# Kernel tuning notes

Hardware: AMD Instinct MI355X
Metric: run time of the kernel (lower is better)

The kernel has to match this reference:

```python
import jax, jax.numpy as jnp
import numpy as np

D = 256; NH = 8; NL = 4; NP = 4; NLAYERS = 6; DFF = 1024; DH = D // NH
B = 2
SHAPES = [(128, 128), (64, 64), (32, 32), (16, 16)]
S_TOTAL = sum(h * w for h, w in SHAPES)  # 21760


def setup_inputs() -> dict:
    key = jax.random.key(0)
    ks = iter(jax.random.split(key, 64))
    inp = {}
    for l, (h, w) in enumerate(SHAPES):
        inp[f"src{l}"] = jax.random.normal(next(ks), (B, D, h, w), jnp.float32)
        inp[f"pos{l}"] = jax.random.normal(next(ks), (B, D, h, w), jnp.float32)
    def p(shape):
        return jax.random.normal(next(ks), shape, jnp.float32) * 0.02
    inp["level_embed"] = p((NL, D))
    inp["Woff"] = p((NLAYERS, D, NH * NL * NP * 2)); inp["boff"] = p((NLAYERS, NH * NL * NP * 2))
    inp["Wattn"] = p((NLAYERS, D, NH * NL * NP)); inp["battn"] = p((NLAYERS, NH * NL * NP))
    inp["Wval"] = p((NLAYERS, D, D)); inp["bval"] = p((NLAYERS, D))
    inp["Wout"] = p((NLAYERS, D, D)); inp["bout"] = p((NLAYERS, D))
    inp["ln1_s"] = jnp.ones((NLAYERS, D)); inp["ln1_b"] = jnp.zeros((NLAYERS, D))
    inp["W1"] = p((NLAYERS, D, DFF)); inp["b1"] = p((NLAYERS, DFF))
    inp["W2"] = p((NLAYERS, DFF, D)); inp["b2"] = p((NLAYERS, D))
    inp["ln2_s"] = jnp.ones((NLAYERS, D)); inp["ln2_b"] = jnp.zeros((NLAYERS, D))
    return inp


def _layer_norm(x, s, b, eps=1e-5):
    m = jnp.mean(x, -1, keepdims=True)
    v = jnp.mean((x - m) ** 2, -1, keepdims=True)
    return (x - m) * jax.lax.rsqrt(v + eps) * s + b


def _ref_points(batch):
    # masks are all-False -> valid_ratios == 1, so reference points are just
    # normalized pixel centers, identical across the level axis.
    refs = []
    for h, w in SHAPES:
        yy, xx = jnp.meshgrid((jnp.arange(h) + 0.5) / h, (jnp.arange(w) + 0.5) / w, indexing="ij")
        refs.append(jnp.stack([xx.ravel(), yy.ravel()], -1))
    ref = jnp.concatenate(refs, 0)  # [S, 2] (x, y)
    return jnp.broadcast_to(ref[None, :, None, :], (batch, S_TOTAL, NL, 2))


def _ms_deform_attn(query, ref, src, Woff, boff, Wattn, battn, Wval, bval, Wout, bout):
    Bq, S, _ = query.shape
    value = (src @ Wval + bval).reshape(Bq, S, NH, DH)
    off = (query @ Woff + boff).reshape(Bq, S, NH, NL, NP, 2)
    aw = jax.nn.softmax((query @ Wattn + battn).reshape(Bq, S, NH, NL * NP), -1)
    aw = aw.reshape(Bq, S, NH, NL, NP)
    norm = jnp.array([[w, h] for h, w in SHAPES], dtype=query.dtype)  # [NL,2] = (W,H)
    loc = ref[:, :, None, :, None, :] + off / norm[None, None, None, :, None, :]  # [B,S,NH,NL,NP,2]
    out = jnp.zeros((Bq, NH, S, DH), query.dtype)
    start = 0
    for l, (h, w) in enumerate(SHAPES):
        v = value[:, start:start + h * w].transpose(0, 2, 1, 3)  # [B,NH,h*w,DH]
        start += h * w
        # grid_sample align_corners=False convention
        x = loc[:, :, :, l, :, 0] * w - 0.5  # [B,S,NH,NP]
        y = loc[:, :, :, l, :, 1] * h - 0.5
        x0 = jnp.floor(x); y0 = jnp.floor(y)
        lx = x - x0; ly = y - y0
        x0i = x0.astype(jnp.int32); y0i = y0.astype(jnp.int32)
        def tr(a):  # [B,S,NH,NP] -> [B,NH,S*NP,1]
            return a.transpose(0, 2, 1, 3).reshape(Bq, NH, S * NP, 1)
        def gather(xi, yi):
            ok = (xi >= 0) & (xi < w) & (yi >= 0) & (yi < h)
            idx = jnp.clip(yi, 0, h - 1) * w + jnp.clip(xi, 0, w - 1)
            idx = idx.transpose(0, 2, 1, 3).reshape(Bq, NH, S * NP)
            g = jnp.take_along_axis(v, idx[..., None], axis=2)  # [B,NH,S*NP,DH]
            return g * tr(ok).astype(v.dtype)  # zero padding outside
        samp = (tr((1 - lx) * (1 - ly)) * gather(x0i, y0i)
                + tr(lx * (1 - ly)) * gather(x0i + 1, y0i)
                + tr((1 - lx) * ly) * gather(x0i, y0i + 1)
                + tr(lx * ly) * gather(x0i + 1, y0i + 1))
        samp = (samp * tr(aw[:, :, :, l])).reshape(Bq, NH, S, NP, DH).sum(3)
        out = out + samp
    out = out.transpose(0, 2, 1, 3).reshape(Bq, S, D)
    return out @ Wout + bout


def _forward(srcs, poss, level_embed, Woff, boff, Wattn, battn, Wval, bval, Wout, bout,
             ln1_s, ln1_b, W1, b1, W2, b2, ln2_s, ln2_b):
    bsz = srcs[0].shape[0]
    src_flat = jnp.concatenate([s.reshape(bsz, D, -1).transpose(0, 2, 1) for s in srcs], 1)
    pos_flat = jnp.concatenate(
        [p.reshape(bsz, D, -1).transpose(0, 2, 1) + level_embed[l] for l, p in enumerate(poss)], 1)
    ref = _ref_points(bsz)
    out = src_flat
    for i in range(NLAYERS):
        q = out + pos_flat
        attn = _ms_deform_attn(q, ref, out, Woff[i], boff[i], Wattn[i], battn[i],
                               Wval[i], bval[i], Wout[i], bout[i])
        out = _layer_norm(out + attn, ln1_s[i], ln1_b[i])
        ff = jax.nn.relu(out @ W1[i] + b1[i]) @ W2[i] + b2[i]
        out = _layer_norm(out + ff, ln2_s[i], ln2_b[i])
    return out  # memory: [B, S_TOTAL, D]


def reference(src0, src1, src2, src3, pos0, pos1, pos2, pos3, level_embed,
              Woff, boff, Wattn, battn, Wval, bval, Wout, bout,
              ln1_s, ln1_b, W1, b1, W2, b2, ln2_s, ln2_b):
    return _forward([src0, src1, src2, src3], [pos0, pos1, pos2, pos3], level_embed,
                    Woff, boff, Wattn, battn, Wval, bval, Wout, bout,
                    ln1_s, ln1_b, W1, b1, W2, b2, ln2_s, ln2_b)
```

## Files before the change

kernel.cpp:

```cpp
#include <hip/hip_runtime.h>
#include <math.h>

#define DMODEL 256
#define NHEADS 8
#define NLAY 6
#define DFF 1024
#define DHEAD 32
#define NB 2
#define STOT 21760
#define MTOT (NB * STOT)

typedef unsigned short u16;
typedef __attribute__((ext_vector_type(8))) short short8;
typedef __attribute__((ext_vector_type(4))) float floatx4;
typedef __attribute__((ext_vector_type(2))) float float2v;

__device__ __forceinline__ float bf2f(u16 h) {
    unsigned int u = ((unsigned int)h) << 16;
    return __uint_as_float(u);
}
__device__ __forceinline__ u16 f2bf(float f) {
    unsigned int u = __float_as_uint(f);
    u = u + 0x7fffu + ((u >> 16) & 1u);
    return (u16)(u >> 16);
}

__device__ __forceinline__ void pkfma(float2v& acc, float2v a, float2v b) {
    asm("v_pk_fma_f32 %0, %1, %2, %0" : "+v"(acc) : "v"(a), "v"(b));
}
__device__ __forceinline__ float2v unpk(unsigned int u) {
    float2v r;
    r.x = __uint_as_float(u << 16);
    r.y = __uint_as_float(u & 0xffff0000u);
    return r;
}

__global__ __launch_bounds__(256)
void biascat_kernel(const float* __restrict__ boff, const float* __restrict__ battn,
                    float* __restrict__ bias384)
{
    const int t = blockIdx.x * 256 + threadIdx.x;
    if (t >= NLAY * 384) return;
    const int i = t / 384, c = t - i * 384;
    bias384[t] = (c < 256) ? boff[i * 256 + c] : battn[i * 128 + (c - 256)];
}

__global__ __launch_bounds__(256)
void wtrans_kernel(const float* __restrict__ W, u16* __restrict__ Wt,
                   const int K, const int N, const long wstride, const long ostride)
{
    __shared__ float ts[32][33];
    W  += blockIdx.z * wstride;
    Wt += blockIdx.z * ostride;
    const int n0 = blockIdx.x * 32;
    const int k0 = blockIdx.y * 32;
    const int t = threadIdx.x;
    const int nl = t & 31, kl = t >> 5;
#pragma unroll
    for (int p = 0; p < 4; ++p) {
        const int k = kl + p * 8;
        ts[k][nl] = W[(long)(k0 + k) * N + n0 + nl];
    }
    __syncthreads();
    const int c = t & 31, r0 = t >> 5;
#pragma unroll
    for (int p = 0; p < 4; ++p) {
        const int r = r0 + p * 8;
        Wt[(long)(n0 + r) * K + k0 + c] = f2bf(ts[c][r]);
    }
}

__global__ __launch_bounds__(256)
void flatten_kernel(const float* __restrict__ src, const float* __restrict__ pos,
                    const float* __restrict__ le_row,
                    float* __restrict__ out, u16* __restrict__ outb,
                    u16* __restrict__ posb, u16* __restrict__ qb,
                    int HW, int start)
{
    __shared__ float ts[32][33];
    __shared__ float tp[32][33];
    const int b   = blockIdx.z;
    const int d0  = blockIdx.y * 32;
    const int hw0 = blockIdx.x * 32;
    const int t   = threadIdx.x;
    const int hwl = t & 31;
    const int dl  = t >> 5;
#pragma unroll
    for (int p = 0; p < 4; ++p) {
        const int dd = dl + p * 8;
        const int d  = d0 + dd;
        const long idx = ((long)(b * DMODEL + d)) * HW + hw0 + hwl;
        ts[dd][hwl] = src[idx];
        tp[dd][hwl] = pos[idx] + le_row[d];
    }
    __syncthreads();
    const int dl2  = t & 31;
    const int hwl2 = t >> 5;
#pragma unroll
    for (int p = 0; p < 4; ++p) {
        const int hh  = hwl2 + p * 8;
        const int tok = start + hw0 + hh;
        const long o  = ((long)(b * STOT + tok)) * DMODEL + d0 + dl2;
        const float v = ts[dl2][hh];
        const float pp = tp[dl2][hh];
        out[o]  = v;
        outb[o] = f2bf(v);
        posb[o] = f2bf(pp);
        qb[o]   = f2bf(v + pp);
    }
}

__global__ __launch_bounds__(256)
void mfma_gemm(const u16* __restrict__ A, const u16* __restrict__ Bt,
               const int ldb, const float* __restrict__ bias,
               u16* __restrict__ Cb, const int ldc, u16* __restrict__ Cb2,
               const int K, const int relu)
{
    __shared__ u16 As[128 * 40];
    __shared__ u16 Bs[128 * 40];
    const int tid  = threadIdx.x;
    const int wv   = tid >> 6;
    const int lane = tid & 63;
    const int m0 = blockIdx.y * 128;
    const int n0 = blockIdx.x * 128;
    const int wm = (wv & 1) * 64;
    const int wn = (wv >> 1) * 64;
    const int q   = lane >> 4;
    const int c16 = lane & 15;

    const int srow = tid >> 2;
    const int scol = (tid & 3) * 8;

    floatx4 acc[4][4];
#pragma unroll
    for (int i = 0; i < 4; ++i)
#pragma unroll
        for (int j = 0; j < 4; ++j)
            acc[i][j] = (floatx4){0.f, 0.f, 0.f, 0.f};

    union Frag { short8 v; uint2 u[2]; };

    for (int k0 = 0; k0 < K; k0 += 32) {
#pragma unroll
        for (int it = 0; it < 2; ++it) {
            const int r = srow + it * 64;
            const uint4 va = *(const uint4*)(A + (long)(m0 + r) * K + k0 + scol);
            uint2 lo, hi;
            lo.x = va.x; lo.y = va.y; hi.x = va.z; hi.y = va.w;
            *(uint2*)&As[r * 40 + scol]     = lo;
            *(uint2*)&As[r * 40 + scol + 4] = hi;
            const uint4 vb = *(const uint4*)(Bt + (long)(n0 + r) * ldb + k0 + scol);
            lo.x = vb.x; lo.y = vb.y; hi.x = vb.z; hi.y = vb.w;
            *(uint2*)&Bs[r * 40 + scol]     = lo;
            *(uint2*)&Bs[r * 40 + scol + 4] = hi;
        }
        __syncthreads();

        short8 af[4], bf[4];
#pragma unroll
        for (int i = 0; i < 4; ++i) {
            Frag fa;
            const int ao = (wm + i * 16 + c16) * 40 + q * 8;
            fa.u[0] = *(const uint2*)&As[ao];
            fa.u[1] = *(const uint2*)&As[ao + 4];
            af[i] = fa.v;
            Frag fb;
            const int bo = (wn + i * 16 + c16) * 40 + q * 8;
            fb.u[0] = *(const uint2*)&Bs[bo];
            fb.u[1] = *(const uint2*)&Bs[bo + 4];
            bf[i] = fb.v;
        }
#pragma unroll
        for (int i = 0; i < 4; ++i)
#pragma unroll
            for (int j = 0; j < 4; ++j)
                acc[i][j] = __builtin_amdgcn_mfma_f32_16x16x32_bf16(
                    af[i], bf[j], acc[i][j], 0, 0, 0);
        __syncthreads();
    }

    u16* cb  = Cb;
    int ldcb = ldc, csub = 0;
    if (Cb2 && n0 >= 256) { cb = Cb2; ldcb = 128; csub = 256; }

#pragma unroll
    for (int i = 0; i < 4; ++i) {
#pragma unroll
        for (int j = 0; j < 4; ++j) {
            const int col = n0 + wn + j * 16 + c16;
            const float bv = bias ? bias[col] : 0.f;
#pragma unroll
            for (int r = 0; r < 4; ++r) {
                const int row = m0 + wm + i * 16 + q * 4 + r;
                float v = acc[i][j][r] + bv;
                if (relu) v = fmaxf(v, 0.f);
                cb[(long)row * ldcb + col - csub] = f2bf(v);
            }
        }
    }
}

__device__ __forceinline__ void point_corners(
    float refx, float refy, unsigned int o2, float aP,
    int k, unsigned int base, float w[4], unsigned int o[4])
{
    const int lw = 128 >> k;
    const float flw = (float)lw;
    const float x = refx * flw - 0.5f + bf2f((u16)(o2 & 0xffffu));
    const float y = refy * flw - 0.5f + bf2f((u16)(o2 >> 16));
    const float x0f = floorf(x), y0f = floorf(y);
    const float lx = x - x0f, ly = y - y0f;
    const int x0 = (int)x0f, y0 = (int)y0f;
    const float wx0 = ((unsigned int)x0 < (unsigned int)lw) ? (1.f - lx) : 0.f;
    const float wx1 = ((unsigned int)(x0 + 1) < (unsigned int)lw) ? lx : 0.f;
    const float wy0 = ((unsigned int)y0 < (unsigned int)lw) ? (aP * (1.f - ly)) : 0.f;
    const float wy1 = ((unsigned int)(y0 + 1) < (unsigned int)lw) ? (aP * ly) : 0.f;
    const unsigned int xc0 = (unsigned int)(x0 & (lw - 1)) << 9;
    const unsigned int xc1 = (unsigned int)((x0 + 1) & (lw - 1)) << 9;
    const unsigned int r0 = (unsigned int)(y0 & (lw - 1)) << (16 - k);
    const unsigned int r1 = (unsigned int)((y0 + 1) & (lw - 1)) << (16 - k);
    w[0] = wy0 * wx0; o[0] = base + r0 + xc0;
    w[1] = wy0 * wx1; o[1] = base + r0 + xc1;
    w[2] = wy1 * wx0; o[2] = base + r1 + xc0;
    w[3] = wy1 * wx1; o[3] = base + r1 + xc1;
}

__device__ __forceinline__ void corner_acc(const char* __restrict__ vp,
                                           unsigned int o, float w,
                                           float2v acc[16])
{
    const uint4 d0 = *(const uint4*)(vp + o);
    const uint4 d1 = *(const uint4*)(vp + o + 16);
    const uint4 d2 = *(const uint4*)(vp + o + 32);
    const uint4 d3 = *(const uint4*)(vp + o + 48);
    float2v w2; w2.x = w; w2.y = w;
    pkfma(acc[0],  w2, unpk(d0.x));
    pkfma(acc[1],  w2, unpk(d0.y));
    pkfma(acc[2],  w2, unpk(d0.z));
    pkfma(acc[3],  w2, unpk(d0.w));
    pkfma(acc[4],  w2, unpk(d1.x));
    pkfma(acc[5],  w2, unpk(d1.y));
    pkfma(acc[6],  w2, unpk(d1.z));
    pkfma(acc[7],  w2, unpk(d1.w));
    pkfma(acc[8],  w2, unpk(d2.x));
    pkfma(acc[9],  w2, unpk(d2.y));
    pkfma(acc[10], w2, unpk(d2.z));
    pkfma(acc[11], w2, unpk(d2.w));
    pkfma(acc[12], w2, unpk(d3.x));
    pkfma(acc[13], w2, unpk(d3.y));
    pkfma(acc[14], w2, unpk(d3.z));
    pkfma(acc[15], w2, unpk(d3.w));
}

__global__ __launch_bounds__(256)
void sample_kernel(const u16* __restrict__ value, const u16* __restrict__ offb,
                   const u16* __restrict__ logit, u16* __restrict__ sb)
{
    __shared__ float red[4][64][33];

    const int t  = threadIdx.x;
    const int wv = t >> 6;
    const int l  = t & 63;
    const int h  = l >> 3;
    const int q  = l & 7;
    const int blk = blockIdx.x * 4 + wv;
    const int b = blk / STOT;
    const int s = blk - b * STOT;

    float refx, refy;
    if (s < 16384) {
        const int yy = s >> 7, xx = s & 127;
        refx = (xx + 0.5f) * (1.f / 128.f); refy = (yy + 0.5f) * (1.f / 128.f);
    } else if (s < 20480) {
        const int sl = s - 16384; const int yy = sl >> 6, xx = sl & 63;
        refx = (xx + 0.5f) * (1.f / 64.f);  refy = (yy + 0.5f) * (1.f / 64.f);
    } else if (s < 21504) {
        const int sl = s - 20480; const int yy = sl >> 5, xx = sl & 31;
        refx = (xx + 0.5f) * (1.f / 32.f);  refy = (yy + 0.5f) * (1.f / 32.f);
    } else {
        const int sl = s - 21504; const int yy = sl >> 4, xx = sl & 15;
        refx = (xx + 0.5f) * (1.f / 16.f);  refy = (yy + 0.5f) * (1.f / 16.f);
    }

    const unsigned int* offp = (const unsigned int*)(offb + (long)blk * 256 + h * 32);
    const unsigned int o2_0 = offp[q];
    const unsigned int o2_1 = offp[q + 8];
    const u16* lp = logit + (long)blk * 128 + h * 16;
    const float l0 = bf2f(lp[q]);
    const float l1 = bf2f(lp[q + 8]);

    float m = fmaxf(l0, l1);
    m = fmaxf(m, __shfl_xor(m, 1));
    m = fmaxf(m, __shfl_xor(m, 2));
    m = fmaxf(m, __shfl_xor(m, 4));
    const float e0 = __expf(l0 - m);
    const float e1 = __expf(l1 - m);
    float se = e0 + e1;
    se += __shfl_xor(se, 1);
    se += __shfl_xor(se, 2);
    se += __shfl_xor(se, 4);
    const float inv = 1.f / se;
    const float aP0 = e0 * inv;
    const float aP1 = e1 * inv;

    const int k0 = q >> 2;
    const int k1 = k0 + 2;
    const unsigned int LS0 = k0 ? 16384u : 0u;
    const unsigned int LS1 = k0 ? 21504u : 20480u;
    const unsigned int tb = (unsigned int)(b * STOT);
    const unsigned int hb64 = (unsigned int)(h * 64);
    const unsigned int base0 = (tb + LS0) * 512u + hb64;
    const unsigned int base1 = (tb + LS1) * 512u + hb64;

    float w0[4], w1[4];
    unsigned int oo0[4], oo1[4];
    point_corners(refx, refy, o2_0, aP0, k0, base0, w0, oo0);
    point_corners(refx, refy, o2_1, aP1, k1, base1, w1, oo1);

    float2v acc[16];
#pragma unroll
    for (int n = 0; n < 16; ++n) { acc[n].x = 0.f; acc[n].y = 0.f; }

    const char* vp = (const char*)value;
#pragma unroll
    for (int c = 0; c < 4; ++c) corner_acc(vp, oo0[c], w0[c], acc);
#pragma unroll
    for (int c = 0; c < 4; ++c) corner_acc(vp, oo1[c], w1[c], acc);

    float* myrow = red[wv][l];
#pragma unroll
    for (int c = 0; c < 8; ++c) {
        float4 v4;
        v4.x = acc[2 * c].x;     v4.y = acc[2 * c].y;
        v4.z = acc[2 * c + 1].x; v4.w = acc[2 * c + 1].y;
        *(float4*)(myrow + c * 4) = v4;
    }
    __builtin_amdgcn_wave_barrier();
    const float* hrow = red[wv][h * 8];
    float4 sum; sum.x = 0.f; sum.y = 0.f; sum.z = 0.f; sum.w = 0.f;
#pragma unroll
    for (int j = 0; j < 8; ++j) {
        const float4 v = *(const float4*)(hrow + j * 33 + q * 4);
        sum.x += v.x; sum.y += v.y; sum.z += v.z; sum.w += v.w;
    }

    ushort4 r;
    r.x = f2bf(sum.x); r.y = f2bf(sum.y); r.z = f2bf(sum.z); r.w = f2bf(sum.w);
    *(ushort4*)(sb + (long)blk * DMODEL + h * 32 + q * 4) = r;
}

__global__ __launch_bounds__(256)
void ln_kernel(float* __restrict__ out, u16* __restrict__ outb,
               u16* __restrict__ qb, const u16* __restrict__ posb,
               const u16* __restrict__ db,
               const float* __restrict__ gamma, const float* __restrict__ beta)
{
    const int wave = threadIdx.x >> 6;
    const int lane = threadIdx.x & 63;
    const long tok = (long)blockIdx.x * 4 + wave;
    float* op = out + tok * DMODEL + lane * 4;
    const float4 xo = *(const float4*)op;
    const ushort4 d4 = *(const ushort4*)(db + tok * DMODEL + lane * 4);
    float x[4] = {xo.x + bf2f(d4.x), xo.y + bf2f(d4.y),
                  xo.z + bf2f(d4.z), xo.w + bf2f(d4.w)};

    float sum = x[0] + x[1] + x[2] + x[3];
#pragma unroll
    for (int o = 32; o >= 1; o >>= 1) sum += __shfl_xor(sum, o);
    const float mean = sum * (1.f / 256.f);

    float vs = 0.f;
#pragma unroll
    for (int i = 0; i < 4; ++i) { const float d2 = x[i] - mean; vs += d2 * d2; }
#pragma unroll
    for (int o = 32; o >= 1; o >>= 1) vs += __shfl_xor(vs, o);
    const float rstd = rsqrtf(vs * (1.f / 256.f) + 1e-5f);

    const float4 g  = *(const float4*)(gamma + lane * 4);
    const float4 be = *(const float4*)(beta + lane * 4);
    float r[4];
    r[0] = (x[0] - mean) * rstd * g.x + be.x;
    r[1] = (x[1] - mean) * rstd * g.y + be.y;
    r[2] = (x[2] - mean) * rstd * g.z + be.z;
    r[3] = (x[3] - mean) * rstd * g.w + be.w;
    float4 rf; rf.x = r[0]; rf.y = r[1]; rf.z = r[2]; rf.w = r[3];
    *(float4*)op = rf;
    ushort4 rb;
    rb.x = f2bf(r[0]); rb.y = f2bf(r[1]); rb.z = f2bf(r[2]); rb.w = f2bf(r[3]);
    *(ushort4*)(outb + tok * DMODEL + lane * 4) = rb;
    if (qb) {
        const ushort4 p4 = *(const ushort4*)(posb + tok * DMODEL + lane * 4);
        ushort4 qv;
        qv.x = f2bf(r[0] + bf2f(p4.x));
        qv.y = f2bf(r[1] + bf2f(p4.y));
        qv.z = f2bf(r[2] + bf2f(p4.z));
        qv.w = f2bf(r[3] + bf2f(p4.w));
        *(ushort4*)(qb + tok * DMODEL + lane * 4) = qv;
    }
}

extern "C" void kernel_launch(void* const* d_in, const int* in_sizes, int n_in,
                              void* d_out, int out_size, void* d_ws, size_t ws_size,
                              hipStream_t stream)
{
    const float* src[4] = {(const float*)d_in[0], (const float*)d_in[2],
                           (const float*)d_in[4], (const float*)d_in[6]};
    const float* pos[4] = {(const float*)d_in[1], (const float*)d_in[3],
                           (const float*)d_in[5], (const float*)d_in[7]};
    const float* level_embed = (const float*)d_in[8];
    const float* Woff  = (const float*)d_in[9];
    const float* boff  = (const float*)d_in[10];
    const float* Wattn = (const float*)d_in[11];
    const float* battn = (const float*)d_in[12];
    const float* Wval  = (const float*)d_in[13];
    const float* bval  = (const float*)d_in[14];
    const float* Wout  = (const float*)d_in[15];
    const float* bout  = (const float*)d_in[16];
    const float* ln1s  = (const float*)d_in[17];
    const float* ln1b  = (const float*)d_in[18];
    const float* W1    = (const float*)d_in[19];
    const float* b1    = (const float*)d_in[20];
    const float* W2    = (const float*)d_in[21];
    const float* b2    = (const float*)d_in[22];
    const float* ln2s  = (const float*)d_in[23];
    const float* ln2b  = (const float*)d_in[24];

    float* out = (float*)d_out;
    const long MD = (long)MTOT * DMODEL;

    u16* outb = (u16*)d_ws;
    u16* posb = outb + MD;
    u16* qb   = posb + MD;
    u16* db   = qb + MD;
    u16* vb   = db + MD;
    u16* offb = vb + MD;
    u16* awb  = offb + MD;
    u16* sb   = awb + MD / 2;
    u16* hb   = vb;
    u16* wts  = vb + 4 * MD;
    u16* Wvalt = wts;
    u16* Wofat = Wvalt + 6L * 256 * 256;
    u16* Woutt = Wofat + 6L * 384 * 256;
    u16* W1t   = Woutt + 6L * 256 * 256;
    u16* W2t   = W1t   + 6L * 1024 * 256;
    float* bias384 = (float*)(W2t + 6L * 1024 * 256);

    biascat_kernel<<<9, 256, 0, stream>>>(boff, battn, bias384);
    wtrans_kernel<<<dim3(8, 8, 6),  256, 0, stream>>>(Wval,  Wvalt, 256, 256,
                                                      65536, 65536);
    wtrans_kernel<<<dim3(8, 8, 6),  256, 0, stream>>>(Woff,  Wofat, 256, 256,
                                                      65536, 98304);
    wtrans_kernel<<<dim3(4, 8, 6),  256, 0, stream>>>(Wattn, Wofat + 256 * 256,
                                                      256, 128, 32768, 98304);
    wtrans_kernel<<<dim3(8, 8, 6),  256, 0, stream>>>(Wout,  Woutt, 256, 256,
                                                      65536, 65536);
    wtrans_kernel<<<dim3(32, 8, 6), 256, 0, stream>>>(W1,    W1t, 256, 1024,
                                                      262144, 262144);
    wtrans_kernel<<<dim3(8, 32, 6), 256, 0, stream>>>(W2,    W2t, 1024, 256,
                                                      262144, 262144);

    {
        const int HW[4] = {16384, 4096, 1024, 256};
        const int ST[4] = {0, 16384, 20480, 21504};
        for (int l = 0; l < 4; ++l) {
            dim3 g(HW[l] / 32, DMODEL / 32, NB);
            flatten_kernel<<<g, 256, 0, stream>>>(src[l], pos[l],
                                                  level_embed + l * DMODEL,
                                                  out, outb, posb, qb, HW[l], ST[l]);
        }
    }

    const dim3 g2(2, MTOT / 128);
    const dim3 g3(3, MTOT / 128);
    const dim3 g8(8, MTOT / 128);

    for (int i = 0; i < NLAY; ++i) {
        const u16* Wv  = Wvalt + (long)i * 256 * 256;
        const u16* Wqa = Wofat + (long)i * 384 * 256;
        const u16* Wou = Woutt + (long)i * 256 * 256;
        const u16* W1i = W1t   + (long)i * 1024 * 256;
        const u16* W2i = W2t   + (long)i * 256 * 1024;
        const float* bv  = bval + (long)i * 256;
        const float* bqa = bias384 + (long)i * 384;
        const float* bou = bout + (long)i * 256;
        const float* b1i = b1   + (long)i * DFF;
        const float* b2i = b2   + (long)i * 256;

        mfma_gemm<<<g2, 256, 0, stream>>>(outb, Wv, 256, bv,
                                          vb, 256, nullptr, 256, 0);
        mfma_gemm<<<g3, 256, 0, stream>>>(qb, Wqa, 256, bqa,
                                          offb, 256, awb, 256, 0);
        sample_kernel<<<MTOT / 4, 256, 0, stream>>>(vb, offb, awb, sb);
        mfma_gemm<<<g2, 256, 0, stream>>>(sb, Wou, 256, bou,
                                          db, 256, nullptr, 256, 0);
        ln_kernel<<<MTOT / 4, 256, 0, stream>>>(out, outb, nullptr, nullptr, db,
                                                ln1s + (long)i * 256,
                                                ln1b + (long)i * 256);
        mfma_gemm<<<g8, 256, 0, stream>>>(outb, W1i, 256, b1i,
                                          hb, 1024, nullptr, 256, 1);
        mfma_gemm<<<g2, 256, 0, stream>>>(hb, W2i, 1024, b2i,
                                          db, 256, nullptr, 1024, 0);
        ln_kernel<<<MTOT / 4, 256, 0, stream>>>(out, outb, qb, posb, db,
                                                ln2s + (long)i * 256,
                                                ln2b + (long)i * 256);
    }
}
```

Measured before the change: 2.139 ms.

## Use direct global-to-LDS loads in GEMM and shuffle-based channel-split sampling

```diff
diff --git a/kernel.cpp b/kernel.cpp
--- a/kernel.cpp
+++ b/kernel.cpp
@@ -33,6 +33,13 @@
     r.x = __uint_as_float(u << 16);
     r.y = __uint_as_float(u & 0xffff0000u);
     return r;
+}
+
+__device__ __forceinline__ void gload16(const u16* g, u16* l) {
+    __builtin_amdgcn_global_load_lds(
+        (const __attribute__((address_space(1))) unsigned int*)(g),
+        (__attribute__((address_space(3))) unsigned int*)(l),
+        16, 0, 0);
 }
 
 __global__ __launch_bounds__(256)
@@ -116,8 +123,8 @@
                u16* __restrict__ Cb, const int ldc, u16* __restrict__ Cb2,
                const int K, const int relu)
 {
-    __shared__ u16 As[128 * 40];
-    __shared__ u16 Bs[128 * 40];
+    __shared__ u16 As[128 * 32];
+    __shared__ u16 Bs[128 * 32];
     const int tid  = threadIdx.x;
     const int wv   = tid >> 6;
     const int lane = tid & 63;
@@ -128,8 +135,18 @@
     const int q   = lane >> 4;
     const int c16 = lane & 15;
 
-    const int srow = tid >> 2;
-    const int scol = (tid & 3) * 8;
+    const int lrow = lane >> 2;
+    const int lcol = (lane & 3) * 8;
+
+    const u16* ag[2];
+    const u16* bg[2];
+#pragma unroll
+    for (int it = 0; it < 2; ++it) {
+        const int chunk = it * 4 + wv;
+        const int row = chunk * 16 + lrow;
+        ag[it] = A  + (long)(m0 + row) * K   + lcol;
+        bg[it] = Bt + (long)(n0 + row) * ldb + lcol;
+    }
 
     floatx4 acc[4][4];
 #pragma unroll
@@ -138,37 +155,20 @@
         for (int j = 0; j < 4; ++j)
             acc[i][j] = (floatx4){0.f, 0.f, 0.f, 0.f};
 
-    union Frag { short8 v; uint2 u[2]; };
-
     for (int k0 = 0; k0 < K; k0 += 32) {
 #pragma unroll
         for (int it = 0; it < 2; ++it) {
-            const int r = srow + it * 64;
-            const uint4 va = *(const uint4*)(A + (long)(m0 + r) * K + k0 + scol);
-            uint2 lo, hi;
-            lo.x = va.x; lo.y = va.y; hi.x = va.z; hi.y = va.w;
-            *(uint2*)&As[r * 40 + scol]     = lo;
-            *(uint2*)&As[r * 40 + scol + 4] = hi;
-            const uint4 vb = *(const uint4*)(Bt + (long)(n0 + r) * ldb + k0 + scol);
-            lo.x = vb.x; lo.y = vb.y; hi.x = vb.z; hi.y = vb.w;
-            *(uint2*)&Bs[r * 40 + scol]     = lo;
-            *(uint2*)&Bs[r * 40 + scol + 4] = hi;
+            const int chunk = it * 4 + wv;
+            gload16(ag[it] + k0, &As[chunk * 512]);
+            gload16(bg[it] + k0, &Bs[chunk * 512]);
         }
         __syncthreads();
 
         short8 af[4], bf[4];
 #pragma unroll
         for (int i = 0; i < 4; ++i) {
-            Frag fa;
-            const int ao = (wm + i * 16 + c16) * 40 + q * 8;
-            fa.u[0] = *(const uint2*)&As[ao];
-            fa.u[1] = *(const uint2*)&As[ao + 4];
-            af[i] = fa.v;
-            Frag fb;
-            const int bo = (wn + i * 16 + c16) * 40 + q * 8;
-            fb.u[0] = *(const uint2*)&Bs[bo];
-            fb.u[1] = *(const uint2*)&Bs[bo + 4];
-            bf[i] = fb.v;
+            af[i] = *(const short8*)&As[(wm + i * 16 + c16) * 32 + q * 8];
+            bf[i] = *(const short8*)&Bs[(wn + i * 16 + c16) * 32 + q * 8];
         }
 #pragma unroll
         for (int i = 0; i < 4; ++i)
@@ -202,7 +202,7 @@
 
 __device__ __forceinline__ void point_corners(
     float refx, float refy, unsigned int o2, float aP,
-    int k, unsigned int base, float w[4], unsigned int o[4])
+    int k, unsigned int base, float* w, unsigned int* o)
 {
     const int lw = 128 >> k;
     const float flw = (float)lw;
@@ -225,44 +225,15 @@
     w[3] = wy1 * wx1; o[3] = base + r1 + xc1;
 }
 
-__device__ __forceinline__ void corner_acc(const char* __restrict__ vp,
-                                           unsigned int o, float w,
-                                           float2v acc[16])
-{
-    const uint4 d0 = *(const uint4*)(vp + o);
-    const uint4 d1 = *(const uint4*)(vp + o + 16);
-    const uint4 d2 = *(const uint4*)(vp + o + 32);
-    const uint4 d3 = *(const uint4*)(vp + o + 48);
-    float2v w2; w2.x = w; w2.y = w;
-    pkfma(acc[0],  w2, unpk(d0.x));
-    pkfma(acc[1],  w2, unpk(d0.y));
-    pkfma(acc[2],  w2, unpk(d0.z));
-    pkfma(acc[3],  w2, unpk(d0.w));
-    pkfma(acc[4],  w2, unpk(d1.x));
-    pkfma(acc[5],  w2, unpk(d1.y));
-    pkfma(acc[6],  w2, unpk(d1.z));
-    pkfma(acc[7],  w2, unpk(d1.w));
-    pkfma(acc[8],  w2, unpk(d2.x));
-    pkfma(acc[9],  w2, unpk(d2.y));
-    pkfma(acc[10], w2, unpk(d2.z));
-    pkfma(acc[11], w2, unpk(d2.w));
-    pkfma(acc[12], w2, unpk(d3.x));
-    pkfma(acc[13], w2, unpk(d3.y));
-    pkfma(acc[14], w2, unpk(d3.z));
-    pkfma(acc[15], w2, unpk(d3.w));
-}
-
-__global__ __launch_bounds__(256)
+__global__ __launch_bounds__(256, 4)
 void sample_kernel(const u16* __restrict__ value, const u16* __restrict__ offb,
                    const u16* __restrict__ logit, u16* __restrict__ sb)
 {
-    __shared__ float red[4][64][33];
-
     const int t  = threadIdx.x;
     const int wv = t >> 6;
     const int l  = t & 63;
     const int h  = l >> 3;
-    const int q  = l & 7;
+    const int u  = l & 7;
     const int blk = blockIdx.x * 4 + wv;
     const int b = blk / STOT;
     const int s = blk - b * STOT;
@@ -283,11 +254,11 @@
     }
 
     const unsigned int* offp = (const unsigned int*)(offb + (long)blk * 256 + h * 32);
-    const unsigned int o2_0 = offp[q];
-    const unsigned int o2_1 = offp[q + 8];
+    const unsigned int o2_0 = offp[u];
+    const unsigned int o2_1 = offp[u + 8];
     const u16* lp = logit + (long)blk * 128 + h * 16;
-    const float l0 = bf2f(lp[q]);
-    const float l1 = bf2f(lp[q + 8]);
+    const float l0 = bf2f(lp[u]);
+    const float l1 = bf2f(lp[u + 8]);
 
     float m = fmaxf(l0, l1);
     m = fmaxf(m, __shfl_xor(m, 1));
@@ -303,8 +274,7 @@
     const float aP0 = e0 * inv;
     const float aP1 = e1 * inv;
 
-    const int k0 = q >> 2;
-    const int k1 = k0 + 2;
+    const int k0 = u >> 2;
     const unsigned int LS0 = k0 ? 16384u : 0u;
     const unsigned int LS1 = k0 ? 21504u : 20480u;
     const unsigned int tb = (unsigned int)(b * STOT);
@@ -312,41 +282,48 @@
     const unsigned int base0 = (tb + LS0) * 512u + hb64;
     const unsigned int base1 = (tb + LS1) * 512u + hb64;
 
-    float w0[4], w1[4];
-    unsigned int oo0[4], oo1[4];
-    point_corners(refx, refy, o2_0, aP0, k0, base0, w0, oo0);
-    point_corners(refx, refy, o2_1, aP1, k1, base1, w1, oo1);
-
-    float2v acc[16];
-#pragma unroll
-    for (int n = 0; n < 16; ++n) { acc[n].x = 0.f; acc[n].y = 0.f; }
-
+    float ww[8];
+    unsigned int oo[8];
+    point_corners(refx, refy, o2_0, aP0, k0,     base0, ww,     oo);
+    point_corners(refx, refy, o2_1, aP1, k0 + 2, base1, ww + 4, oo + 4);
+
+    const int sbase = l & 56;
+    const unsigned int chb = (unsigned int)(u * 8);
     const char* vp = (const char*)value;
-#pragma unroll
-    for (int c = 0; c < 4; ++c) corner_acc(vp, oo0[c], w0[c], acc);
-#pragma unroll
-    for (int c = 0; c < 4; ++c) corner_acc(vp, oo1[c], w1[c], acc);
-
-    float* myrow = red[wv][l];
-#pragma unroll
-    for (int c = 0; c < 8; ++c) {
-        float4 v4;
-        v4.x = acc[2 * c].x;     v4.y = acc[2 * c].y;
-        v4.z = acc[2 * c + 1].x; v4.w = acc[2 * c + 1].y;
-        *(float4*)(myrow + c * 4) = v4;
-    }
-    __builtin_amdgcn_wave_barrier();
-    const float* hrow = red[wv][h * 8];
-    float4 sum; sum.x = 0.f; sum.y = 0.f; sum.z = 0.f; sum.w = 0.f;
-#pragma unroll
-    for (int j = 0; j < 8; ++j) {
-        const float4 v = *(const float4*)(hrow + j * 33 + q * 4);
-        sum.x += v.x; sum.y += v.y; sum.z += v.z; sum.w += v.w;
+    float2v acc0; acc0.x = 0.f; acc0.y = 0.f;
+    float2v acc1; acc1.x = 0.f; acc1.y = 0.f;
+
+#pragma unroll
+    for (int g = 0; g < 4; ++g) {
+        float wB[16];
+        unsigned int oB[16];
+        uint2 dB[16];
+#pragma unroll
+        for (int pp = 0; pp < 4; ++pp) {
+            const int p = g * 4 + pp;
+            const int src = sbase + (p & 7);
+            const int slotbase = (p >> 3) * 4;
+#pragma unroll
+            for (int c = 0; c < 4; ++c) {
+                oB[pp * 4 + c] = (unsigned int)__shfl((int)oo[slotbase + c], src);
+                wB[pp * 4 + c] = __shfl(ww[slotbase + c], src);
+            }
+        }
+#pragma unroll
+        for (int i = 0; i < 16; ++i)
+            dB[i] = *(const uint2*)(vp + (oB[i] + chb));
+#pragma unroll
+        for (int i = 0; i < 16; ++i) {
+            float2v w2; w2.x = wB[i]; w2.y = wB[i];
+            pkfma(acc0, w2, unpk(dB[i].x));
+            pkfma(acc1, w2, unpk(dB[i].y));
+        }
     }
 
     ushort4 r;
-    r.x = f2bf(sum.x); r.y = f2bf(sum.y); r.z = f2bf(sum.z); r.w = f2bf(sum.w);
-    *(ushort4*)(sb + (long)blk * DMODEL + h * 32 + q * 4) = r;
+    r.x = f2bf(acc0.x); r.y = f2bf(acc0.y);
+    r.z = f2bf(acc1.x); r.w = f2bf(acc1.y);
+    *(ushort4*)(sb + (long)blk * DMODEL + h * 32 + u * 4) = r;
 }
 
 __global__ __launch_bounds__(256)
```

Result: faster. 1.997 ms (-6.6%).
